# Performance work log

Measured on AMD Instinct MI355X. Metric: run time of the kernel, lower is better.

The kernel has to match this reference:

```python
import jax, jax.numpy as jnp
import numpy as np

N, E, D = 50000, 300000, 64
EPS = 0.0  # eps buffer, train_eps=False


def setup_inputs() -> dict:
    key = jax.random.key(0)
    ks = jax.random.split(key, 24)
    inp = {}
    i = 0
    for d in range(3):
        inp[f"x{d}"] = jax.random.normal(ks[i], (N, D), jnp.float32); i += 1
        inp[f"up_index{d}"] = jax.random.randint(ks[i], (2, E), 0, N, jnp.int32); i += 1
        inp[f"down_index{d}"] = jax.random.randint(ks[i], (2, E), 0, N, jnp.int32); i += 1
        inp[f"up_attr{d}"] = jax.random.normal(ks[i], (E, D), jnp.float32); i += 1
        inp[f"down_attr{d}"] = jax.random.normal(ks[i], (E, D), jnp.float32); i += 1
    s2 = 1.0 / np.sqrt(2 * D)
    s1 = 1.0 / np.sqrt(D)
    inp["W_up"] = jax.random.normal(ks[i], (2 * D, D), jnp.float32) * s2; i += 1
    inp["b_up"] = jnp.zeros((D,), jnp.float32)
    inp["W_down"] = jax.random.normal(ks[i], (2 * D, D), jnp.float32) * s2; i += 1
    inp["b_down"] = jnp.zeros((D,), jnp.float32)
    inp["W1"] = jax.random.normal(ks[i], (D, D), jnp.float32) * s1; i += 1
    inp["b1"] = jnp.zeros((D,), jnp.float32)
    inp["W2"] = jax.random.normal(ks[i], (D, D), jnp.float32) * s1; i += 1
    inp["b2"] = jnp.zeros((D,), jnp.float32)
    return inp


def _level(x, up_idx, down_idx, up_attr, down_attr,
           W_up, b_up, W_down, b_down, W1, b1, W2, b2):
    # message_up: gather source feats, concat attr, MLP, scatter-add to targets
    m_up = jax.nn.relu(jnp.concatenate([x[up_idx[1]], up_attr], axis=-1) @ W_up + b_up)
    out_up = jax.ops.segment_sum(m_up, up_idx[0], num_segments=N)
    m_dn = jax.nn.relu(jnp.concatenate([x[down_idx[1]], down_attr], axis=-1) @ W_down + b_down)
    out_dn = jax.ops.segment_sum(m_dn, down_idx[0], num_segments=N)
    # out_up += (1+eps)x; out_down += (1+eps)x; update(out_up + out_down)
    h = out_up + out_dn + (2.0 * (1.0 + EPS)) * x
    return jax.nn.relu(jax.nn.relu(h @ W1 + b1) @ W2 + b2)


def reference(x0, up_index0, down_index0, up_attr0, down_attr0,
              x1, up_index1, down_index1, up_attr1, down_attr1,
              x2, up_index2, down_index2, up_attr2, down_attr2,
              W_up, b_up, W_down, b_down, W1, b1, W2, b2):
    params = (W_up, b_up, W_down, b_down, W1, b1, W2, b2)
    o0 = _level(x0, up_index0, down_index0, up_attr0, down_attr0, *params)
    o1 = _level(x1, up_index1, down_index1, up_attr1, down_attr1, *params)
    o2 = _level(x2, up_index2, down_index2, up_attr2, down_attr2, *params)
    return (o0, o1, o2)
```

## Files before the change

kernel.cpp:

```cpp
#include <hip/hip_runtime.h>
#include <hip/hip_fp16.h>

#define NN 50000
#define NE 300000
#define ETILES (NE / 16)
#define NTILES (NN / 16)
#define WLDS_STRIDE 136

typedef _Float16 f16;
typedef _Float16 f16x4 __attribute__((ext_vector_type(4)));
typedef _Float16 f16x8 __attribute__((ext_vector_type(8)));
typedef float f32x4 __attribute__((ext_vector_type(4)));

struct Idx6 { const int* p[6]; };

__device__ __forceinline__ f16x4 cvt4(float4 v) {
    f16x4 r; r.x = (f16)v.x; r.y = (f16)v.y; r.z = (f16)v.z; r.w = (f16)v.w;
    return r;
}

__global__ void init2_kernel(const float* __restrict__ x0, const float* __restrict__ x1,
                             const float* __restrict__ x2,
                             f16* __restrict__ hbase, f16* __restrict__ xhbase) {
    const size_t i = (size_t)blockIdx.x * 256 + threadIdx.x;
    const int lvl = (int)(i / (NN * 16));
    const size_t li = i - (size_t)lvl * (NN * 16);
    const float* xs = (lvl == 0) ? x0 : (lvl == 1) ? x1 : x2;
    float4 v = ((const float4*)xs)[li];
    f16x4 xo, ho;
    xo.x = (f16)v.x;        xo.y = (f16)v.y;        xo.z = (f16)v.z;        xo.w = (f16)v.w;
    ho.x = (f16)(2.f*v.x);  ho.y = (f16)(2.f*v.y);  ho.z = (f16)(2.f*v.z);  ho.w = (f16)(2.f*v.w);
    ((f16x4*)(xhbase + (size_t)lvl * NN * 64))[li] = xo;
    ((f16x4*)(hbase  + (size_t)lvl * NN * 64))[li] = ho;
}

__global__ void wtrans_kernel(const float* __restrict__ WU, const float* __restrict__ WD,
                              f16* __restrict__ WtU, f16* __restrict__ WtD) {
    const int i = blockIdx.x * 256 + threadIdx.x;
    const int k = i >> 6, c = i & 63;
    WtU[c * 128 + k] = (f16)WU[i];
    WtD[c * 128 + k] = (f16)WD[i];
}

__global__ void zero_cnt_kernel(int* __restrict__ cnt) {
    const int i = blockIdx.x * 256 + threadIdx.x;
    if (i < 6 * NN) cnt[i] = 0;
}

__global__ void hist_kernel(Idx6 idx, int* __restrict__ cnt) {
    const int e = blockIdx.x * 256 + threadIdx.x;
    const int d = blockIdx.y;
    if (e < NE) atomicAdd(&cnt[d * NN + idx.p[d][e]], 1);
}

__device__ __forceinline__ int block_incl_scan(int v, int tid, int* sb) {
    sb[tid] = v; __syncthreads();
#pragma unroll
    for (int off = 1; off < 256; off <<= 1) {
        int t = (tid >= off) ? sb[tid - off] : 0;
        __syncthreads();
        sb[tid] += t;
        __syncthreads();
    }
    return sb[tid];
}

__global__ void scan1_kernel(const int* __restrict__ cnt, int* __restrict__ rptmp,
                             int* __restrict__ bsum) {
    __shared__ int sb[256];
    const int d = blockIdx.y, tid = threadIdx.x;
    const int i = blockIdx.x * 256 + tid;
    const int v = (i < NN) ? cnt[d * NN + i] : 0;
    const int incl = block_incl_scan(v, tid, sb);
    if (i < NN) rptmp[d * NN + i] = incl - v;
    if (tid == 255) bsum[d * 256 + blockIdx.x] = incl;
}

__global__ void scan2_kernel(int* __restrict__ bsum) {
    __shared__ int sb[256];
    const int d = blockIdx.x, tid = threadIdx.x;
    const int v = (tid < 196) ? bsum[d * 256 + tid] : 0;
    const int incl = block_incl_scan(v, tid, sb);
    bsum[d * 256 + tid] = incl - v;
}

__global__ void scan3_kernel(const int* __restrict__ cnt, const int* __restrict__ rptmp,
                             const int* __restrict__ bsum,
                             int* __restrict__ rowptr, int* __restrict__ cursor) {
    const int d = blockIdx.y;
    const int i = blockIdx.x * 256 + threadIdx.x;
    if (i < NN) {
        const int v = rptmp[d * NN + i] + bsum[d * 256 + blockIdx.x];
        rowptr[d * (NN + 1) + i] = v;
        cursor[d * NN + i] = v;
        if (i == NN - 1) rowptr[d * (NN + 1) + NN] = v + cnt[d * NN + i];
    }
}

__global__ void scatter_kernel(Idx6 idx, int* __restrict__ cursor, int* __restrict__ pos) {
    const int e = blockIdx.x * 256 + threadIdx.x;
    const int d = blockIdx.y;
    if (e < NE) pos[(size_t)d * NE + e] = atomicAdd(&cursor[d * NN + idx.p[d][e]], 1);
}

__global__ __launch_bounds__(256) void edge_mlp_kernel(
    const f16* __restrict__ xh,
    const int* __restrict__ ui, const int* __restrict__ di,
    const float* __restrict__ ua, const float* __restrict__ da,
    const f16* __restrict__ WtU, const f16* __restrict__ WtD,
    const float* __restrict__ bU, const float* __restrict__ bD,
    const int* __restrict__ posU, const int* __restrict__ posD,
    __half* __restrict__ mU, __half* __restrict__ mD) {

    __shared__ __align__(16) f16 Wlds[64 * WLDS_STRIDE];

    const int dir = blockIdx.y;
    const int* __restrict__ idx    = dir ? di : ui;
    const float* __restrict__ attr = dir ? da : ua;
    const f16* __restrict__ Wt     = dir ? WtD : WtU;
    const float* __restrict__ b    = dir ? bD : bU;
    const int* __restrict__ pos    = dir ? posD : posU;
    __half* __restrict__ m         = dir ? mD : mU;

    const int tt   = threadIdx.x;
    const int lane = tt & 63;
    const int wid  = tt >> 6;
    const int lr   = lane & 15;
    const int lg   = (lane >> 4) & 3;

    for (int i = tt; i < 1024; i += 256) {
        const int row = i >> 4, seg = i & 15;
        *(f16x8*)&Wlds[row * WLDS_STRIDE + seg * 8] = *(const f16x8*)&Wt[row * 128 + seg * 8];
    }
    float bf[4];
#pragma unroll
    for (int n = 0; n < 4; ++n) bf[n] = b[n * 16 + lr];
    __syncthreads();

    const int tile = blockIdx.x * 4 + wid;
    if (tile >= ETILES) return;
    const int e0 = tile << 4;

    const int src = idx[NE + e0 + lr];
    const int pv  = pos[e0 + lr];

    const float4* a4 = (const float4*)attr;

    f16x4 afr[8];
#pragma unroll
    for (int k0 = 0; k0 < 4; ++k0)
        afr[k0] = *(const f16x4*)&xh[(size_t)src * 64 + k0 * 16 + 4 * lg];
#pragma unroll
    for (int k0 = 0; k0 < 4; ++k0)
        afr[4 + k0] = cvt4(a4[(size_t)(e0 + lr) * 16 + 4 * k0 + lg]);

    f32x4 acc[4];
#pragma unroll
    for (int n = 0; n < 4; ++n) acc[n] = (f32x4){0.f, 0.f, 0.f, 0.f};
#pragma unroll
    for (int k0 = 0; k0 < 8; ++k0) {
#pragma unroll
        for (int n = 0; n < 4; ++n) {
            const f16x4 wf = *(const f16x4*)&Wlds[(n * 16 + lr) * WLDS_STRIDE + k0 * 16 + 4 * lg];
            acc[n] = __builtin_amdgcn_mfma_f32_16x16x16f16(afr[k0], wf, acc[n], 0, 0, 0);
        }
    }

#pragma unroll
    for (int j = 0; j < 4; ++j) {
        float v[4], vn[4];
#pragma unroll
        for (int n = 0; n < 4; ++n) v[n] = fmaxf(acc[n][j] + bf[n], 0.f);
#pragma unroll
        for (int n = 0; n < 4; ++n) vn[n] = __shfl_xor(v[n], 1);
        const int s = __shfl(pv, 4 * lg + j);
        __half* mp = m + (size_t)s * 64;
        if ((lane & 1) == 0) {
            *(__half2*)(mp + 0 * 16 + lr) = __floats2half2_rn(v[0], vn[0]);
            *(__half2*)(mp + 1 * 16 + lr) = __floats2half2_rn(v[1], vn[1]);
        } else {
            *(__half2*)(mp + 2 * 16 + lr - 1) = __floats2half2_rn(vn[2], v[2]);
            *(__half2*)(mp + 3 * 16 + lr - 1) = __floats2half2_rn(vn[3], v[3]);
        }
    }
}

__global__ __launch_bounds__(256) void agg_kernel(
    const float* __restrict__ x,
    const __half* __restrict__ mU, const __half* __restrict__ mD,
    const int* __restrict__ rpU, const int* __restrict__ rpD,
    f16* __restrict__ agg) {

    const int tid  = threadIdx.x;
    const int node = blockIdx.x * 16 + (tid >> 4);
    const int c4   = tid & 15;

    float4 xv = ((const float4*)x)[(size_t)node * 16 + c4];
    float a0 = 2.f * xv.x, a1 = 2.f * xv.y, a2 = 2.f * xv.z, a3 = 2.f * xv.w;

    {
        const int beg = rpU[node], end = rpU[node + 1];
        for (int k = beg; k < end; ++k) {
            f16x4 mv = *(const f16x4*)((const f16*)mU + (size_t)k * 64 + c4 * 4);
            a0 += (float)mv.x; a1 += (float)mv.y; a2 += (float)mv.z; a3 += (float)mv.w;
        }
    }
    {
        const int beg = rpD[node], end = rpD[node + 1];
        for (int k = beg; k < end; ++k) {
            f16x4 mv = *(const f16x4*)((const f16*)mD + (size_t)k * 64 + c4 * 4);
            a0 += (float)mv.x; a1 += (float)mv.y; a2 += (float)mv.z; a3 += (float)mv.w;
        }
    }
    f16x4 o; o.x = (f16)a0; o.y = (f16)a1; o.z = (f16)a2; o.w = (f16)a3;
    *(f16x4*)&agg[(size_t)node * 64 + c4 * 4] = o;
}

__device__ __forceinline__ int ld_comb(const int* __restrict__ idx, int tile, int l5) {
    const int e0 = tile << 4;
    return idx[(l5 < 16) ? (NE + e0 + l5) : (e0 + l5 - 16)];
}

__global__ __launch_bounds__(256) void edge4_kernel(
    const f16* __restrict__ xh,
    const int* __restrict__ ui, const int* __restrict__ di,
    const float* __restrict__ ua, const float* __restrict__ da,
    const f16* __restrict__ WtU, const f16* __restrict__ WtD,
    const float* __restrict__ bU, const float* __restrict__ bD,
    __half* __restrict__ h) {

    __shared__ __align__(16) f16 Wlds[64 * WLDS_STRIDE];

    const int dir = blockIdx.y;
    const int* __restrict__ idx    = dir ? di : ui;
    const float* __restrict__ attr = dir ? da : ua;
    const f16* __restrict__ Wt     = dir ? WtD : WtU;
    const float* __restrict__ b    = dir ? bD : bU;

    const int tt   = threadIdx.x;
    const int lane = tt & 63;
    const int wid  = tt >> 6;
    const int lr   = lane & 15;
    const int lg   = (lane >> 4) & 3;
    const int l5   = lane & 31;

    for (int i = tt; i < 1024; i += 256) {
        const int row = i >> 4, seg = i & 15;
        *(f16x8*)&Wlds[row * WLDS_STRIDE + seg * 8] = *(const f16x8*)&Wt[row * 128 + seg * 8];
    }
    float bf[4];
#pragma unroll
    for (int n = 0; n < 4; ++n) bf[n] = b[n * 16 + lr];
    __syncthreads();

    const float4* a4 = (const float4*)attr;
    const int S = gridDim.x * 4;
    int t = blockIdx.x * 4 + wid;
    if (t >= ETILES) return;

    for (; t < ETILES; t += S) {
        const int e0 = t << 4;
        const int cA = ld_comb(idx, t, l5);
        const int src = __shfl(cA, lr);
        int tg[4];
#pragma unroll
        for (int j = 0; j < 4; ++j) tg[j] = __shfl(cA, 16 + 4 * lg + j);

        f16x4 afr[8];
#pragma unroll
        for (int k0 = 0; k0 < 4; ++k0)
            afr[k0] = *(const f16x4*)&xh[(size_t)src * 64 + k0 * 16 + 4 * lg];
#pragma unroll
        for (int k0 = 0; k0 < 4; ++k0)
            afr[4 + k0] = cvt4(a4[(size_t)(e0 + lr) * 16 + 4 * k0 + lg]);

        f32x4 acc[4];
#pragma unroll
        for (int n = 0; n < 4; ++n) acc[n] = (f32x4){0.f, 0.f, 0.f, 0.f};
#pragma unroll
        for (int k0 = 0; k0 < 8; ++k0)
#pragma unroll
            for (int n = 0; n < 4; ++n) {
                const f16x4 wf = *(const f16x4*)&Wlds[(n * 16 + lr) * WLDS_STRIDE + k0 * 16 + 4 * lg];
                acc[n] = __builtin_amdgcn_mfma_f32_16x16x16f16(afr[k0], wf, acc[n], 0, 0, 0);
            }

#pragma unroll
        for (int j = 0; j < 4; ++j) {
            float v[4], vn[4];
#pragma unroll
            for (int n = 0; n < 4; ++n) v[n] = fmaxf(acc[n][j] + bf[n], 0.f);
#pragma unroll
            for (int n = 0; n < 4; ++n) vn[n] = __shfl_xor(v[n], 1);
            __half* hp = h + (size_t)tg[j] * 64;
            if ((lane & 1) == 0) {
                unsafeAtomicAdd((__half2*)(hp + 0 * 16 + lr), __floats2half2_rn(v[0], vn[0]));
                unsafeAtomicAdd((__half2*)(hp + 1 * 16 + lr), __floats2half2_rn(v[1], vn[1]));
            } else {
                unsafeAtomicAdd((__half2*)(hp + 2 * 16 + lr - 1), __floats2half2_rn(vn[2], v[2]));
                unsafeAtomicAdd((__half2*)(hp + 3 * 16 + lr - 1), __floats2half2_rn(vn[3], v[3]));
            }
        }
    }
}

__global__ __launch_bounds__(256) void node_kernel(
    const f16* __restrict__ hbase, float* __restrict__ outb,
    const float* __restrict__ W1, const float* __restrict__ b1,
    const float* __restrict__ W2, const float* __restrict__ b2) {

    __shared__ f16 Y[4][16 * 72];

    const int t    = threadIdx.x;
    const int lane = t & 63;
    const int wid  = t >> 6;
    const int lr   = lane & 15;
    const int lg   = (lane >> 4) & 3;

    f16x4 w1f[4][4], w2f[4][4];
#pragma unroll
    for (int k0 = 0; k0 < 4; ++k0) {
        const int kb = k0 * 16 + 4 * lg;
#pragma unroll
        for (int n = 0; n < 4; ++n) {
            const int c = n * 16 + lr;
            f16x4 w;
            w.x = (f16)W1[(kb + 0) * 64 + c];
            w.y = (f16)W1[(kb + 1) * 64 + c];
            w.z = (f16)W1[(kb + 2) * 64 + c];
            w.w = (f16)W1[(kb + 3) * 64 + c];
            w1f[k0][n] = w;
            w.x = (f16)W2[(kb + 0) * 64 + c];
            w.y = (f16)W2[(kb + 1) * 64 + c];
            w.z = (f16)W2[(kb + 2) * 64 + c];
            w.w = (f16)W2[(kb + 3) * 64 + c];
            w2f[k0][n] = w;
        }
    }
    float b1f[4], b2f[4];
#pragma unroll
    for (int n = 0; n < 4; ++n) {
        b1f[n] = b1[n * 16 + lr];
        b2f[n] = b2[n * 16 + lr];
    }

    const int gw     = blockIdx.x * 4 + wid;
    const int stride = gridDim.x * 4;
    for (int tile = gw; tile < 3 * NTILES; tile += stride) {
        const int lvl = tile / NTILES;
        const int n0  = (tile - lvl * NTILES) << 4;
        float* out = outb + (size_t)lvl * NN * 64;
        const f16* h16 = hbase + (size_t)lvl * NN * 64;

        f16x4 a[4];
#pragma unroll
        for (int k0 = 0; k0 < 4; ++k0)
            a[k0] = *(const f16x4*)&h16[(size_t)(n0 + lr) * 64 + k0 * 16 + 4 * lg];

        f32x4 acc[4];
#pragma unroll
        for (int n = 0; n < 4; ++n) acc[n] = (f32x4){0.f, 0.f, 0.f, 0.f};
#pragma unroll
        for (int k0 = 0; k0 < 4; ++k0)
#pragma unroll
            for (int n = 0; n < 4; ++n)
                acc[n] = __builtin_amdgcn_mfma_f32_16x16x16f16(a[k0], w1f[k0][n], acc[n], 0, 0, 0);

#pragma unroll
        for (int n = 0; n < 4; ++n)
#pragma unroll
            for (int j = 0; j < 4; ++j) {
                float v = acc[n][j] + b1f[n];
                v = v > 0.f ? v : 0.f;
                Y[wid][(4 * lg + j) * 72 + n * 16 + lr] = (f16)v;
            }

        f16x4 a2[4];
#pragma unroll
        for (int k0 = 0; k0 < 4; ++k0)
            a2[k0] = *(const f16x4*)&Y[wid][lr * 72 + k0 * 16 + 4 * lg];

        f32x4 acc2[4];
#pragma unroll
        for (int n = 0; n < 4; ++n) acc2[n] = (f32x4){0.f, 0.f, 0.f, 0.f};
#pragma unroll
        for (int k0 = 0; k0 < 4; ++k0)
#pragma unroll
            for (int n = 0; n < 4; ++n)
                acc2[n] = __builtin_amdgcn_mfma_f32_16x16x16f16(a2[k0], w2f[k0][n], acc2[n], 0, 0, 0);

#pragma unroll
        for (int n = 0; n < 4; ++n)
#pragma unroll
            for (int j = 0; j < 4; ++j) {
                float v = acc2[n][j] + b2f[n];
                v = v > 0.f ? v : 0.f;
                out[(size_t)(n0 + 4 * lg + j) * 64 + n * 16 + lr] = v;
            }
    }
}

extern "C" void kernel_launch(void* const* d_in, const int* in_sizes, int n_in,
                              void* d_out, int out_size, void* d_ws, size_t ws_size,
                              hipStream_t stream) {
    (void)in_sizes; (void)n_in; (void)out_size;

    const float* W_up   = (const float*)d_in[15];
    const float* b_up   = (const float*)d_in[16];
    const float* W_down = (const float*)d_in[17];
    const float* b_down = (const float*)d_in[18];
    const float* W1     = (const float*)d_in[19];
    const float* b1     = (const float*)d_in[20];
    const float* W2     = (const float*)d_in[21];
    const float* b2     = (const float*)d_in[22];

    const float* x0 = (const float*)d_in[0];
    const float* x1 = (const float*)d_in[5];
    const float* x2 = (const float*)d_in[10];

    size_t off = 0;
    auto alloc = [&](size_t bytes) { size_t o = off; off = (off + bytes + 255) & ~(size_t)255; return o; };
    const size_t o_xh   = alloc((size_t)3 * NN * 64 * 2);
    const size_t o_agg  = alloc((size_t)3 * NN * 64 * 2);
    const size_t o_wt   = alloc((size_t)2 * 128 * 64 * 2);
    const size_t fallback_need = off;
    const size_t o_m    = alloc((size_t)2 * NE * 64 * 2);
    const size_t o_pos  = alloc((size_t)6 * NE * 4);
    const size_t o_rp   = alloc((size_t)6 * (NN + 1) * 4);
    const size_t o_cur  = alloc((size_t)6 * NN * 4);
    const size_t o_rpt  = alloc((size_t)6 * NN * 4);
    const size_t o_bsum = alloc((size_t)6 * 256 * 4);
    const size_t o_cnt  = alloc((size_t)6 * NN * 4);
    const size_t full_need = off;

    char* ws = (char*)d_ws;
    f16*  xh   = (f16*)(ws + o_xh);
    f16*  agg  = (f16*)(ws + o_agg);
    f16*  WtU  = (f16*)(ws + o_wt);
    f16*  WtD  = WtU + 128 * 64;

    if (ws_size >= full_need) {
        __half* mU  = (__half*)(ws + o_m);
        __half* mD  = mU + (size_t)NE * 64;
        int* pos    = (int*)(ws + o_pos);
        int* rowptr = (int*)(ws + o_rp);
        int* cursor = (int*)(ws + o_cur);
        int* rptmp  = (int*)(ws + o_rpt);
        int* bsum   = (int*)(ws + o_bsum);
        int* cnt    = (int*)(ws + o_cnt);

        Idx6 idx;
        for (int d = 0; d < 3; ++d) {
            idx.p[2 * d + 0] = (const int*)d_in[5 * d + 1];
            idx.p[2 * d + 1] = (const int*)d_in[5 * d + 2];
        }

        zero_cnt_kernel<<<1172, 256, 0, stream>>>(cnt);
        hist_kernel<<<dim3(1172, 6), 256, 0, stream>>>(idx, cnt);
        scan1_kernel<<<dim3(196, 6), 256, 0, stream>>>(cnt, rptmp, bsum);
        scan2_kernel<<<6, 256, 0, stream>>>(bsum);
        scan3_kernel<<<dim3(196, 6), 256, 0, stream>>>(cnt, rptmp, bsum, rowptr, cursor);
        scatter_kernel<<<dim3(1172, 6), 256, 0, stream>>>(idx, cursor, pos);

        wtrans_kernel<<<32, 256, 0, stream>>>(W_up, W_down, WtU, WtD);
        init2_kernel<<<9375, 256, 0, stream>>>(x0, x1, x2, agg, xh);

        for (int d = 0; d < 3; ++d) {
            const float* x  = (const float*)d_in[5 * d + 0];
            const int*   ui = (const int*)  d_in[5 * d + 1];
            const int*   di = (const int*)  d_in[5 * d + 2];
            const float* ua = (const float*)d_in[5 * d + 3];
            const float* da = (const float*)d_in[5 * d + 4];
            const f16* xhd = xh + (size_t)d * NN * 64;
            edge_mlp_kernel<<<dim3(4688, 2), 256, 0, stream>>>(
                xhd, ui, di, ua, da, WtU, WtD, b_up, b_down,
                pos + (size_t)(2 * d) * NE, pos + (size_t)(2 * d + 1) * NE, mU, mD);
            agg_kernel<<<3125, 256, 0, stream>>>(
                x, mU, mD,
                rowptr + (size_t)(2 * d) * (NN + 1), rowptr + (size_t)(2 * d + 1) * (NN + 1),
                agg + (size_t)d * NN * 64);
        }
        node_kernel<<<586, 256, 0, stream>>>(agg, (float*)d_out, W1, b1, W2, b2);
    } else if (ws_size >= fallback_need) {
        wtrans_kernel<<<32, 256, 0, stream>>>(W_up, W_down, WtU, WtD);
        init2_kernel<<<9375, 256, 0, stream>>>(x0, x1, x2, agg, xh);
        for (int d = 0; d < 3; ++d) {
            const int*   ui = (const int*)  d_in[5 * d + 1];
            const int*   di = (const int*)  d_in[5 * d + 2];
            const float* ua = (const float*)d_in[5 * d + 3];
            const float* da = (const float*)d_in[5 * d + 4];
            const f16* xhd = xh + (size_t)d * NN * 64;
            __half* h = (__half*)(agg + (size_t)d * NN * 64);
            edge4_kernel<<<dim3(1024, 2), 256, 0, stream>>>(
                xhd, ui, di, ua, da, WtU, WtD, b_up, b_down, h);
        }
        node_kernel<<<586, 256, 0, stream>>>(agg, (float*)d_out, W1, b1, W2, b2);
    }
}
```

Measured before the change: 476.0 us.

## Write edge messages in natural order, gather via sorted edge ids, fuse aggregation with node MLP

The edge MLP kernel now writes messages contiguously in edge order and processes two 16-edge tiles per wave, instead of scattering each row to a CSR-sorted position. The aggregation gathers messages through a sorted edge-id list and is fused with the two-layer node MLP per level, which removes the f16 agg buffer round trip and the separate node kernel. Edge writes become coalesced, but the aggregation reads become indirect random gathers with an extra index load per edge. The aggnode grid is also smaller, so fewer waves are available to hide gather latency.

```diff
diff --git a/kernel.cpp b/kernel.cpp
--- a/kernel.cpp
+++ b/kernel.cpp
@@ -6,6 +6,7 @@
 #define ETILES (NE / 16)
 #define NTILES (NN / 16)
 #define WLDS_STRIDE 136
+#define ASTR 68
 
 typedef _Float16 f16;
 typedef _Float16 f16x4 __attribute__((ext_vector_type(4)));
@@ -17,6 +18,16 @@
 __device__ __forceinline__ f16x4 cvt4(float4 v) {
     f16x4 r; r.x = (f16)v.x; r.y = (f16)v.y; r.z = (f16)v.z; r.w = (f16)v.w;
     return r;
+}
+
+__global__ void init_xh_kernel(const float* __restrict__ x0, const float* __restrict__ x1,
+                               const float* __restrict__ x2, f16* __restrict__ xhbase) {
+    const size_t i = (size_t)blockIdx.x * 256 + threadIdx.x;
+    const int lvl = (int)(i / (NN * 16));
+    const size_t li = i - (size_t)lvl * (NN * 16);
+    const float* xs = (lvl == 0) ? x0 : (lvl == 1) ? x1 : x2;
+    float4 v = ((const float4*)xs)[li];
+    ((f16x4*)(xhbase + (size_t)lvl * NN * 64))[li] = cvt4(v);
 }
 
 __global__ void init2_kernel(const float* __restrict__ x0, const float* __restrict__ x1,
@@ -97,19 +108,21 @@
     }
 }
 
-__global__ void scatter_kernel(Idx6 idx, int* __restrict__ cursor, int* __restrict__ pos) {
+__global__ void scatter_eids_kernel(Idx6 idx, int* __restrict__ cursor, int* __restrict__ eids) {
     const int e = blockIdx.x * 256 + threadIdx.x;
     const int d = blockIdx.y;
-    if (e < NE) pos[(size_t)d * NE + e] = atomicAdd(&cursor[d * NN + idx.p[d][e]], 1);
-}
-
-__global__ __launch_bounds__(256) void edge_mlp_kernel(
+    if (e < NE) {
+        const int p = atomicAdd(&cursor[d * NN + idx.p[d][e]], 1);
+        eids[(size_t)d * NE + p] = e;
+    }
+}
+
+__global__ __launch_bounds__(256) void edge_nat_kernel(
     const f16* __restrict__ xh,
     const int* __restrict__ ui, const int* __restrict__ di,
     const float* __restrict__ ua, const float* __restrict__ da,
     const f16* __restrict__ WtU, const f16* __restrict__ WtD,
     const float* __restrict__ bU, const float* __restrict__ bD,
-    const int* __restrict__ posU, const int* __restrict__ posD,
     __half* __restrict__ mU, __half* __restrict__ mD) {
 
     __shared__ __align__(16) f16 Wlds[64 * WLDS_STRIDE];
@@ -119,7 +132,6 @@
     const float* __restrict__ attr = dir ? da : ua;
     const f16* __restrict__ Wt     = dir ? WtD : WtU;
     const float* __restrict__ b    = dir ? bD : bU;
-    const int* __restrict__ pos    = dir ? posD : posU;
     __half* __restrict__ m         = dir ? mD : mU;
 
     const int tt   = threadIdx.x;
@@ -128,192 +140,87 @@
     const int lr   = lane & 15;
     const int lg   = (lane >> 4) & 3;
 
-    for (int i = tt; i < 1024; i += 256) {
-        const int row = i >> 4, seg = i & 15;
-        *(f16x8*)&Wlds[row * WLDS_STRIDE + seg * 8] = *(const f16x8*)&Wt[row * 128 + seg * 8];
+    for (int i = tt; i < 2048; i += 256) {
+        const int row = i >> 5, seg = i & 31;
+        *(f16x4*)&Wlds[row * WLDS_STRIDE + seg * 4] = *(const f16x4*)&Wt[row * 128 + seg * 4];
     }
     float bf[4];
 #pragma unroll
     for (int n = 0; n < 4; ++n) bf[n] = b[n * 16 + lr];
     __syncthreads();
 
-    const int tile = blockIdx.x * 4 + wid;
-    if (tile >= ETILES) return;
-    const int e0 = tile << 4;
-
-    const int src = idx[NE + e0 + lr];
-    const int pv  = pos[e0 + lr];
+    const int tp = blockIdx.x * 4 + wid;
+    if (tp * 2 >= ETILES) return;
+    const int e0 = tp << 5;
+
+    const int srcA = idx[NE + e0 + lr];
+    const int srcB = idx[NE + e0 + 16 + lr];
 
     const float4* a4 = (const float4*)attr;
 
-    f16x4 afr[8];
-#pragma unroll
-    for (int k0 = 0; k0 < 4; ++k0)
-        afr[k0] = *(const f16x4*)&xh[(size_t)src * 64 + k0 * 16 + 4 * lg];
-#pragma unroll
-    for (int k0 = 0; k0 < 4; ++k0)
-        afr[4 + k0] = cvt4(a4[(size_t)(e0 + lr) * 16 + 4 * k0 + lg]);
-
-    f32x4 acc[4];
-#pragma unroll
-    for (int n = 0; n < 4; ++n) acc[n] = (f32x4){0.f, 0.f, 0.f, 0.f};
+    f16x4 fA[8], fB[8];
+#pragma unroll
+    for (int k0 = 0; k0 < 4; ++k0) {
+        fA[k0] = *(const f16x4*)&xh[(size_t)srcA * 64 + k0 * 16 + 4 * lg];
+        fB[k0] = *(const f16x4*)&xh[(size_t)srcB * 64 + k0 * 16 + 4 * lg];
+    }
+#pragma unroll
+    for (int k0 = 0; k0 < 4; ++k0) {
+        fA[4 + k0] = cvt4(a4[(size_t)(e0 + lr) * 16 + 4 * k0 + lg]);
+        fB[4 + k0] = cvt4(a4[(size_t)(e0 + 16 + lr) * 16 + 4 * k0 + lg]);
+    }
+
+    f32x4 accA[4], accB[4];
+#pragma unroll
+    for (int n = 0; n < 4; ++n) { accA[n] = (f32x4){0,0,0,0}; accB[n] = (f32x4){0,0,0,0}; }
 #pragma unroll
     for (int k0 = 0; k0 < 8; ++k0) {
 #pragma unroll
         for (int n = 0; n < 4; ++n) {
             const f16x4 wf = *(const f16x4*)&Wlds[(n * 16 + lr) * WLDS_STRIDE + k0 * 16 + 4 * lg];
-            acc[n] = __builtin_amdgcn_mfma_f32_16x16x16f16(afr[k0], wf, acc[n], 0, 0, 0);
-        }
-    }
-
-#pragma unroll
-    for (int j = 0; j < 4; ++j) {
-        float v[4], vn[4];
-#pragma unroll
-        for (int n = 0; n < 4; ++n) v[n] = fmaxf(acc[n][j] + bf[n], 0.f);
-#pragma unroll
-        for (int n = 0; n < 4; ++n) vn[n] = __shfl_xor(v[n], 1);
-        const int s = __shfl(pv, 4 * lg + j);
-        __half* mp = m + (size_t)s * 64;
-        if ((lane & 1) == 0) {
-            *(__half2*)(mp + 0 * 16 + lr) = __floats2half2_rn(v[0], vn[0]);
-            *(__half2*)(mp + 1 * 16 + lr) = __floats2half2_rn(v[1], vn[1]);
-        } else {
-            *(__half2*)(mp + 2 * 16 + lr - 1) = __floats2half2_rn(vn[2], v[2]);
-            *(__half2*)(mp + 3 * 16 + lr - 1) = __floats2half2_rn(vn[3], v[3]);
-        }
-    }
-}
-
-__global__ __launch_bounds__(256) void agg_kernel(
+            accA[n] = __builtin_amdgcn_mfma_f32_16x16x16f16(fA[k0], wf, accA[n], 0, 0, 0);
+            accB[n] = __builtin_amdgcn_mfma_f32_16x16x16f16(fB[k0], wf, accB[n], 0, 0, 0);
+        }
+    }
+
+#pragma unroll
+    for (int tb = 0; tb < 2; ++tb) {
+        const f32x4* acc = tb ? accB : accA;
+        const int eb = e0 + tb * 16;
+#pragma unroll
+        for (int j = 0; j < 4; ++j) {
+            float v[4], vn[4];
+#pragma unroll
+            for (int n = 0; n < 4; ++n) v[n] = fmaxf(acc[n][j] + bf[n], 0.f);
+#pragma unroll
+            for (int n = 0; n < 4; ++n) vn[n] = __shfl_xor(v[n], 1);
+            __half* mp = m + (size_t)(eb + 4 * lg + j) * 64;
+            if ((lane & 1) == 0) {
+                *(__half2*)(mp + 0 * 16 + lr) = __floats2half2_rn(v[0], vn[0]);
+                *(__half2*)(mp + 1 * 16 + lr) = __floats2half2_rn(v[1], vn[1]);
+            } else {
+                *(__half2*)(mp + 2 * 16 + lr - 1) = __floats2half2_rn(vn[2], v[2]);
+                *(__half2*)(mp + 3 * 16 + lr - 1) = __floats2half2_rn(vn[3], v[3]);
+            }
+        }
+    }
+}
+
+__global__ __launch_bounds__(256) void aggnode_kernel(
     const float* __restrict__ x,
     const __half* __restrict__ mU, const __half* __restrict__ mD,
     const int* __restrict__ rpU, const int* __restrict__ rpD,
-    f16* __restrict__ agg) {
-
-    const int tid  = threadIdx.x;
-    const int node = blockIdx.x * 16 + (tid >> 4);
-    const int c4   = tid & 15;
-
-    float4 xv = ((const float4*)x)[(size_t)node * 16 + c4];
-    float a0 = 2.f * xv.x, a1 = 2.f * xv.y, a2 = 2.f * xv.z, a3 = 2.f * xv.w;
-
-    {
-        const int beg = rpU[node], end = rpU[node + 1];
-        for (int k = beg; k < end; ++k) {
-            f16x4 mv = *(const f16x4*)((const f16*)mU + (size_t)k * 64 + c4 * 4);
-            a0 += (float)mv.x; a1 += (float)mv.y; a2 += (float)mv.z; a3 += (float)mv.w;
-        }
-    }
-    {
-        const int beg = rpD[node], end = rpD[node + 1];
-        for (int k = beg; k < end; ++k) {
-            f16x4 mv = *(const f16x4*)((const f16*)mD + (size_t)k * 64 + c4 * 4);
-            a0 += (float)mv.x; a1 += (float)mv.y; a2 += (float)mv.z; a3 += (float)mv.w;
-        }
-    }
-    f16x4 o; o.x = (f16)a0; o.y = (f16)a1; o.z = (f16)a2; o.w = (f16)a3;
-    *(f16x4*)&agg[(size_t)node * 64 + c4 * 4] = o;
-}
-
-__device__ __forceinline__ int ld_comb(const int* __restrict__ idx, int tile, int l5) {
-    const int e0 = tile << 4;
-    return idx[(l5 < 16) ? (NE + e0 + l5) : (e0 + l5 - 16)];
-}
-
-__global__ __launch_bounds__(256) void edge4_kernel(
-    const f16* __restrict__ xh,
-    const int* __restrict__ ui, const int* __restrict__ di,
-    const float* __restrict__ ua, const float* __restrict__ da,
-    const f16* __restrict__ WtU, const f16* __restrict__ WtD,
-    const float* __restrict__ bU, const float* __restrict__ bD,
-    __half* __restrict__ h) {
-
-    __shared__ __align__(16) f16 Wlds[64 * WLDS_STRIDE];
-
-    const int dir = blockIdx.y;
-    const int* __restrict__ idx    = dir ? di : ui;
-    const float* __restrict__ attr = dir ? da : ua;
-    const f16* __restrict__ Wt     = dir ? WtD : WtU;
-    const float* __restrict__ b    = dir ? bD : bU;
+    const int* __restrict__ eU, const int* __restrict__ eD,
+    const float* __restrict__ W1, const float* __restrict__ b1,
+    const float* __restrict__ W2, const float* __restrict__ b2,
+    float* __restrict__ out) {
+
+    __shared__ f16 Ash[4][16 * ASTR];
+    __shared__ f16 Y[4][16 * 72];
 
     const int tt   = threadIdx.x;
     const int lane = tt & 63;
     const int wid  = tt >> 6;
-    const int lr   = lane & 15;
-    const int lg   = (lane >> 4) & 3;
-    const int l5   = lane & 31;
-
-    for (int i = tt; i < 1024; i += 256) {
-        const int row = i >> 4, seg = i & 15;
-        *(f16x8*)&Wlds[row * WLDS_STRIDE + seg * 8] = *(const f16x8*)&Wt[row * 128 + seg * 8];
-    }
-    float bf[4];
-#pragma unroll
-    for (int n = 0; n < 4; ++n) bf[n] = b[n * 16 + lr];
-    __syncthreads();
-
-    const float4* a4 = (const float4*)attr;
-    const int S = gridDim.x * 4;
-    int t = blockIdx.x * 4 + wid;
-    if (t >= ETILES) return;
-
-    for (; t < ETILES; t += S) {
-        const int e0 = t << 4;
-        const int cA = ld_comb(idx, t, l5);
-        const int src = __shfl(cA, lr);
-        int tg[4];
-#pragma unroll
-        for (int j = 0; j < 4; ++j) tg[j] = __shfl(cA, 16 + 4 * lg + j);
-
-        f16x4 afr[8];
-#pragma unroll
-        for (int k0 = 0; k0 < 4; ++k0)
-            afr[k0] = *(const f16x4*)&xh[(size_t)src * 64 + k0 * 16 + 4 * lg];
-#pragma unroll
-        for (int k0 = 0; k0 < 4; ++k0)
-            afr[4 + k0] = cvt4(a4[(size_t)(e0 + lr) * 16 + 4 * k0 + lg]);
-
-        f32x4 acc[4];
-#pragma unroll
-        for (int n = 0; n < 4; ++n) acc[n] = (f32x4){0.f, 0.f, 0.f, 0.f};
-#pragma unroll
-        for (int k0 = 0; k0 < 8; ++k0)
-#pragma unroll
-            for (int n = 0; n < 4; ++n) {
-                const f16x4 wf = *(const f16x4*)&Wlds[(n * 16 + lr) * WLDS_STRIDE + k0 * 16 + 4 * lg];
-                acc[n] = __builtin_amdgcn_mfma_f32_16x16x16f16(afr[k0], wf, acc[n], 0, 0, 0);
-            }
-
-#pragma unroll
-        for (int j = 0; j < 4; ++j) {
-            float v[4], vn[4];
-#pragma unroll
-            for (int n = 0; n < 4; ++n) v[n] = fmaxf(acc[n][j] + bf[n], 0.f);
-#pragma unroll
-            for (int n = 0; n < 4; ++n) vn[n] = __shfl_xor(v[n], 1);
-            __half* hp = h + (size_t)tg[j] * 64;
-            if ((lane & 1) == 0) {
-                unsafeAtomicAdd((__half2*)(hp + 0 * 16 + lr), __floats2half2_rn(v[0], vn[0]));
-                unsafeAtomicAdd((__half2*)(hp + 1 * 16 + lr), __floats2half2_rn(v[1], vn[1]));
-            } else {
-                unsafeAtomicAdd((__half2*)(hp + 2 * 16 + lr - 1), __floats2half2_rn(vn[2], v[2]));
-                unsafeAtomicAdd((__half2*)(hp + 3 * 16 + lr - 1), __floats2half2_rn(vn[3], v[3]));
-            }
-        }
-    }
-}
-
-__global__ __launch_bounds__(256) void node_kernel(
-    const f16* __restrict__ hbase, float* __restrict__ outb,
-    const float* __restrict__ W1, const float* __restrict__ b1,
-    const float* __restrict__ W2, const float* __restrict__ b2) {
-
-    __shared__ f16 Y[4][16 * 72];
-
-    const int t    = threadIdx.x;
-    const int lane = t & 63;
-    const int wid  = t >> 6;
     const int lr   = lane & 15;
     const int lg   = (lane >> 4) & 3;
 
@@ -344,6 +251,215 @@
         b2f[n] = b2[n * 16 + lr];
     }
 
+    const int base = blockIdx.x * 64 + wid * 16;
+
+    const f16* mU16 = (const f16*)mU;
+    const f16* mD16 = (const f16*)mD;
+#pragma unroll
+    for (int r = 0; r < 4; ++r) {
+        const int nl   = 4 * r + lg;
+        const int node = base + nl;
+        float s0 = 0.f, s1 = 0.f, s2 = 0.f, s3 = 0.f;
+        if (node < NN) {
+            float4 xv = ((const float4*)x)[(size_t)node * 16 + lr];
+            s0 = 2.f * xv.x; s1 = 2.f * xv.y; s2 = 2.f * xv.z; s3 = 2.f * xv.w;
+            {
+                const int beg = rpU[node], end = rpU[node + 1];
+                for (int k = beg; k < end; ++k) {
+                    const int e = eU[k];
+                    f16x4 mv = *(const f16x4*)&mU16[(size_t)e * 64 + lr * 4];
+                    s0 += (float)mv.x; s1 += (float)mv.y; s2 += (float)mv.z; s3 += (float)mv.w;
+                }
+            }
+            {
+                const int beg = rpD[node], end = rpD[node + 1];
+                for (int k = beg; k < end; ++k) {
+                    const int e = eD[k];
+                    f16x4 mv = *(const f16x4*)&mD16[(size_t)e * 64 + lr * 4];
+                    s0 += (float)mv.x; s1 += (float)mv.y; s2 += (float)mv.z; s3 += (float)mv.w;
+                }
+            }
+        }
+        f16x4 o; o.x = (f16)s0; o.y = (f16)s1; o.z = (f16)s2; o.w = (f16)s3;
+        *(f16x4*)&Ash[wid][nl * ASTR + lr * 4] = o;
+    }
+
+    f16x4 a[4];
+#pragma unroll
+    for (int k0 = 0; k0 < 4; ++k0)
+        a[k0] = *(const f16x4*)&Ash[wid][lr * ASTR + k0 * 16 + 4 * lg];
+
+    f32x4 acc[4];
+#pragma unroll
+    for (int n = 0; n < 4; ++n) acc[n] = (f32x4){0,0,0,0};
+#pragma unroll
+    for (int k0 = 0; k0 < 4; ++k0)
+#pragma unroll
+        for (int n = 0; n < 4; ++n)
+            acc[n] = __builtin_amdgcn_mfma_f32_16x16x16f16(a[k0], w1f[k0][n], acc[n], 0, 0, 0);
+
+#pragma unroll
+    for (int n = 0; n < 4; ++n)
+#pragma unroll
+        for (int j = 0; j < 4; ++j) {
+            float v = acc[n][j] + b1f[n];
+            v = v > 0.f ? v : 0.f;
+            Y[wid][(4 * lg + j) * 72 + n * 16 + lr] = (f16)v;
+        }
+
+    f16x4 a2[4];
+#pragma unroll
+    for (int k0 = 0; k0 < 4; ++k0)
+        a2[k0] = *(const f16x4*)&Y[wid][lr * 72 + k0 * 16 + 4 * lg];
+
+    f32x4 acc2[4];
+#pragma unroll
+    for (int n = 0; n < 4; ++n) acc2[n] = (f32x4){0,0,0,0};
+#pragma unroll
+    for (int k0 = 0; k0 < 4; ++k0)
+#pragma unroll
+        for (int n = 0; n < 4; ++n)
+            acc2[n] = __builtin_amdgcn_mfma_f32_16x16x16f16(a2[k0], w2f[k0][n], acc2[n], 0, 0, 0);
+
+#pragma unroll
+    for (int n = 0; n < 4; ++n)
+#pragma unroll
+        for (int j = 0; j < 4; ++j) {
+            const int node = base + 4 * lg + j;
+            float v = acc2[n][j] + b2f[n];
+            v = v > 0.f ? v : 0.f;
+            if (node < NN) out[(size_t)node * 64 + n * 16 + lr] = v;
+        }
+}
+
+__device__ __forceinline__ int ld_comb(const int* __restrict__ idx, int tile, int l5) {
+    const int e0 = tile << 4;
+    return idx[(l5 < 16) ? (NE + e0 + l5) : (e0 + l5 - 16)];
+}
+
+__global__ __launch_bounds__(256) void edge4_kernel(
+    const f16* __restrict__ xh,
+    const int* __restrict__ ui, const int* __restrict__ di,
+    const float* __restrict__ ua, const float* __restrict__ da,
+    const f16* __restrict__ WtU, const f16* __restrict__ WtD,
+    const float* __restrict__ bU, const float* __restrict__ bD,
+    __half* __restrict__ h) {
+
+    __shared__ __align__(16) f16 Wlds[64 * WLDS_STRIDE];
+
+    const int dir = blockIdx.y;
+    const int* __restrict__ idx    = dir ? di : ui;
+    const float* __restrict__ attr = dir ? da : ua;
+    const f16* __restrict__ Wt     = dir ? WtD : WtU;
+    const float* __restrict__ b    = dir ? bD : bU;
+
+    const int tt   = threadIdx.x;
+    const int lane = tt & 63;
+    const int wid  = tt >> 6;
+    const int lr   = lane & 15;
+    const int lg   = (lane >> 4) & 3;
+    const int l5   = lane & 31;
+
+    for (int i = tt; i < 2048; i += 256) {
+        const int row = i >> 5, seg = i & 31;
+        *(f16x4*)&Wlds[row * WLDS_STRIDE + seg * 4] = *(const f16x4*)&Wt[row * 128 + seg * 4];
+    }
+    float bf[4];
+#pragma unroll
+    for (int n = 0; n < 4; ++n) bf[n] = b[n * 16 + lr];
+    __syncthreads();
+
+    const float4* a4 = (const float4*)attr;
+    const int S = gridDim.x * 4;
+    int t = blockIdx.x * 4 + wid;
+    if (t >= ETILES) return;
+
+    for (; t < ETILES; t += S) {
+        const int e0 = t << 4;
+        const int cA = ld_comb(idx, t, l5);
+        const int src = __shfl(cA, lr);
+        int tg[4];
+#pragma unroll
+        for (int j = 0; j < 4; ++j) tg[j] = __shfl(cA, 16 + 4 * lg + j);
+
+        f16x4 afr[8];
+#pragma unroll
+        for (int k0 = 0; k0 < 4; ++k0)
+            afr[k0] = *(const f16x4*)&xh[(size_t)src * 64 + k0 * 16 + 4 * lg];
+#pragma unroll
+        for (int k0 = 0; k0 < 4; ++k0)
+            afr[4 + k0] = cvt4(a4[(size_t)(e0 + lr) * 16 + 4 * k0 + lg]);
+
+        f32x4 acc[4];
+#pragma unroll
+        for (int n = 0; n < 4; ++n) acc[n] = (f32x4){0,0,0,0};
+#pragma unroll
+        for (int k0 = 0; k0 < 8; ++k0)
+#pragma unroll
+            for (int n = 0; n < 4; ++n) {
+                const f16x4 wf = *(const f16x4*)&Wlds[(n * 16 + lr) * WLDS_STRIDE + k0 * 16 + 4 * lg];
+                acc[n] = __builtin_amdgcn_mfma_f32_16x16x16f16(afr[k0], wf, acc[n], 0, 0, 0);
+            }
+
+#pragma unroll
+        for (int j = 0; j < 4; ++j) {
+            float v[4], vn[4];
+#pragma unroll
+            for (int n = 0; n < 4; ++n) v[n] = fmaxf(acc[n][j] + bf[n], 0.f);
+#pragma unroll
+            for (int n = 0; n < 4; ++n) vn[n] = __shfl_xor(v[n], 1);
+            __half* hp = h + (size_t)tg[j] * 64;
+            if ((lane & 1) == 0) {
+                unsafeAtomicAdd((__half2*)(hp + 0 * 16 + lr), __floats2half2_rn(v[0], vn[0]));
+                unsafeAtomicAdd((__half2*)(hp + 1 * 16 + lr), __floats2half2_rn(v[1], vn[1]));
+            } else {
+                unsafeAtomicAdd((__half2*)(hp + 2 * 16 + lr - 1), __floats2half2_rn(vn[2], v[2]));
+                unsafeAtomicAdd((__half2*)(hp + 3 * 16 + lr - 1), __floats2half2_rn(vn[3], v[3]));
+            }
+        }
+    }
+}
+
+__global__ __launch_bounds__(256) void node_kernel(
+    const f16* __restrict__ hbase, float* __restrict__ outb,
+    const float* __restrict__ W1, const float* __restrict__ b1,
+    const float* __restrict__ W2, const float* __restrict__ b2) {
+
+    __shared__ f16 Y[4][16 * 72];
+
+    const int t    = threadIdx.x;
+    const int lane = t & 63;
+    const int wid  = t >> 6;
+    const int lr   = lane & 15;
+    const int lg   = (lane >> 4) & 3;
+
+    f16x4 w1f[4][4], w2f[4][4];
+#pragma unroll
+    for (int k0 = 0; k0 < 4; ++k0) {
+        const int kb = k0 * 16 + 4 * lg;
+#pragma unroll
+        for (int n = 0; n < 4; ++n) {
+            const int c = n * 16 + lr;
+            f16x4 w;
+            w.x = (f16)W1[(kb + 0) * 64 + c];
+            w.y = (f16)W1[(kb + 1) * 64 + c];
+            w.z = (f16)W1[(kb + 2) * 64 + c];
+            w.w = (f16)W1[(kb + 3) * 64 + c];
+            w1f[k0][n] = w;
+            w.x = (f16)W2[(kb + 0) * 64 + c];
+            w.y = (f16)W2[(kb + 1) * 64 + c];
+            w.z = (f16)W2[(kb + 2) * 64 + c];
+            w.w = (f16)W2[(kb + 3) * 64 + c];
+            w2f[k0][n] = w;
+        }
+    }
+    float b1f[4], b2f[4];
+#pragma unroll
+    for (int n = 0; n < 4; ++n) {
+        b1f[n] = b1[n * 16 + lr];
+        b2f[n] = b2[n * 16 + lr];
+    }
+
     const int gw     = blockIdx.x * 4 + wid;
     const int stride = gridDim.x * 4;
     for (int tile = gw; tile < 3 * NTILES; tile += stride) {
@@ -359,7 +475,7 @@
 
         f32x4 acc[4];
 #pragma unroll
-        for (int n = 0; n < 4; ++n) acc[n] = (f32x4){0.f, 0.f, 0.f, 0.f};
+        for (int n = 0; n < 4; ++n) acc[n] = (f32x4){0,0,0,0};
 #pragma unroll
         for (int k0 = 0; k0 < 4; ++k0)
 #pragma unroll
@@ -382,7 +498,7 @@
 
         f32x4 acc2[4];
 #pragma unroll
-        for (int n = 0; n < 4; ++n) acc2[n] = (f32x4){0.f, 0.f, 0.f, 0.f};
+        for (int n = 0; n < 4; ++n) acc2[n] = (f32x4){0,0,0,0};
 #pragma unroll
         for (int k0 = 0; k0 < 4; ++k0)
 #pragma unroll
@@ -425,7 +541,7 @@
     const size_t o_wt   = alloc((size_t)2 * 128 * 64 * 2);
     const size_t fallback_need = off;
     const size_t o_m    = alloc((size_t)2 * NE * 64 * 2);
-    const size_t o_pos  = alloc((size_t)6 * NE * 4);
+    const size_t o_eid  = alloc((size_t)6 * NE * 4);
     const size_t o_rp   = alloc((size_t)6 * (NN + 1) * 4);
     const size_t o_cur  = alloc((size_t)6 * NN * 4);
     const size_t o_rpt  = alloc((size_t)6 * NN * 4);
@@ -442,7 +558,7 @@
     if (ws_size >= full_need) {
         __half* mU  = (__half*)(ws + o_m);
         __half* mD  = mU + (size_t)NE * 64;
-        int* pos    = (int*)(ws + o_pos);
+        int* eids   = (int*)(ws + o_eid);
         int* rowptr = (int*)(ws + o_rp);
         int* cursor = (int*)(ws + o_cur);
         int* rptmp  = (int*)(ws + o_rpt);
@@ -455,15 +571,15 @@
             idx.p[2 * d + 1] = (const int*)d_in[5 * d + 2];
         }
 
+        wtrans_kernel<<<32, 256, 0, stream>>>(W_up, W_down, WtU, WtD);
+        init_xh_kernel<<<9375, 256, 0, stream>>>(x0, x1, x2, xh);
+
         zero_cnt_kernel<<<1172, 256, 0, stream>>>(cnt);
         hist_kernel<<<dim3(1172, 6), 256, 0, stream>>>(idx, cnt);
         scan1_kernel<<<dim3(196, 6), 256, 0, stream>>>(cnt, rptmp, bsum);
         scan2_kernel<<<6, 256, 0, stream>>>(bsum);
         scan3_kernel<<<dim3(196, 6), 256, 0, stream>>>(cnt, rptmp, bsum, rowptr, cursor);
-        scatter_kernel<<<dim3(1172, 6), 256, 0, stream>>>(idx, cursor, pos);
-
-        wtrans_kernel<<<32, 256, 0, stream>>>(W_up, W_down, WtU, WtD);
-        init2_kernel<<<9375, 256, 0, stream>>>(x0, x1, x2, agg, xh);
+        scatter_eids_kernel<<<dim3(1172, 6), 256, 0, stream>>>(idx, cursor, eids);
 
         for (int d = 0; d < 3; ++d) {
             const float* x  = (const float*)d_in[5 * d + 0];
@@ -472,15 +588,15 @@
             const float* ua = (const float*)d_in[5 * d + 3];
             const float* da = (const float*)d_in[5 * d + 4];
             const f16* xhd = xh + (size_t)d * NN * 64;
-            edge_mlp_kernel<<<dim3(4688, 2), 256, 0, stream>>>(
-                xhd, ui, di, ua, da, WtU, WtD, b_up, b_down,
-                pos + (size_t)(2 * d) * NE, pos + (size_t)(2 * d + 1) * NE, mU, mD);
-            agg_kernel<<<3125, 256, 0, stream>>>(
+            edge_nat_kernel<<<dim3(2344, 2), 256, 0, stream>>>(
+                xhd, ui, di, ua, da, WtU, WtD, b_up, b_down, mU, mD);
+            aggnode_kernel<<<782, 256, 0, stream>>>(
                 x, mU, mD,
                 rowptr + (size_t)(2 * d) * (NN + 1), rowptr + (size_t)(2 * d + 1) * (NN + 1),
-                agg + (size_t)d * NN * 64);
-        }
-        node_kernel<<<586, 256, 0, stream>>>(agg, (float*)d_out, W1, b1, W2, b2);
+                eids + (size_t)(2 * d) * NE, eids + (size_t)(2 * d + 1) * NE,
+                W1, b1, W2, b2,
+                (float*)d_out + (size_t)d * NN * 64);
+        }
     } else if (ws_size >= fallback_need) {
         wtrans_kernel<<<32, 256, 0, stream>>>(W_up, W_down, WtU, WtD);
         init2_kernel<<<9375, 256, 0, stream>>>(x0, x1, x2, agg, xh);
```

Result: slower. 739.4 us (+55.3%).
